# Performance work log

Measured on AMD Instinct MI355X. Metric: run time of the kernel, lower is better.

## Reference

```python
import jax, jax.numpy as jnp
import numpy as np
from jax.ops import segment_sum

N_NODES = 50000
N_EDGES = 800000
HIDDEN = 96
N_CLASSES = 10
N_GRAPHS = 64


def gcn_conv(x, W, b, src, dst, num_nodes):
    """PyG GCNConv: symmetric-normalized aggregation with self-loops.
    out = D^{-1/2} (A + I) D^{-1/2} (x W) + b, with D the degree of A + I.
    Self-loop contribution handled analytically instead of appending edges.
    """
    ones = jnp.ones((src.shape[0],), dtype=x.dtype)
    deg = segment_sum(ones, dst, num_segments=num_nodes) + 1.0  # +1 for self-loop
    dinv = jax.lax.rsqrt(deg)
    h = x @ W  # [N, H] small GEMM
    norm = dinv[src] * dinv[dst]  # [E]
    msg = h[src] * norm[:, None]  # [E, H] dominant gather
    out = segment_sum(msg, dst, num_segments=num_nodes)  # scatter-add
    out = out + h * (dinv * dinv)[:, None]  # self-loop term
    return out + b


def setup_inputs() -> dict:
    key = jax.random.key(0)
    ks = jax.random.split(key, 12)
    x = jax.random.normal(ks[0], (N_NODES, HIDDEN), dtype=jnp.float32)
    edge_index = jax.random.randint(ks[1], (2, N_EDGES), 0, N_NODES, dtype=jnp.int64)
    batch = jnp.sort(jax.random.randint(ks[2], (N_NODES,), 0, N_GRAPHS, dtype=jnp.int64))
    s = 1.0 / np.sqrt(HIDDEN)
    W0 = jax.random.normal(ks[3], (HIDDEN, HIDDEN), dtype=jnp.float32) * s
    b0 = jnp.zeros((HIDDEN,), dtype=jnp.float32)
    W1 = jax.random.normal(ks[4], (HIDDEN, HIDDEN), dtype=jnp.float32) * s
    b1 = jnp.zeros((HIDDEN,), dtype=jnp.float32)
    W2 = jax.random.normal(ks[5], (HIDDEN, HIDDEN), dtype=jnp.float32) * s
    b2 = jnp.zeros((HIDDEN,), dtype=jnp.float32)
    W_lin = jax.random.normal(ks[6], (HIDDEN, N_CLASSES), dtype=jnp.float32) * s
    b_lin = jnp.zeros((N_CLASSES,), dtype=jnp.float32)
    return {"x": x, "edge_index": edge_index, "batch": batch,
            "W0": W0, "b0": b0, "W1": W1, "b1": b1, "W2": W2, "b2": b2,
            "W_lin": W_lin, "b_lin": b_lin}


def reference(x, edge_index, batch, W0, b0, W1, b1, W2, b2, W_lin, b_lin):
    src, dst = edge_index[0], edge_index[1]
    n = x.shape[0]
    h = jax.nn.relu(gcn_conv(x, W0, b0, src, dst, n))
    h = jax.nn.relu(gcn_conv(h, W1, b1, src, dst, n))
    h = gcn_conv(h, W2, b2, src, dst, n)  # last layer: no activation
    # global_mean_pool over batch index
    sums = segment_sum(h, batch, num_segments=N_GRAPHS)  # [G, H]
    cnts = segment_sum(jnp.ones((n,), dtype=h.dtype), batch, num_segments=N_GRAPHS)
    pooled = sums / jnp.maximum(cnts, 1.0)[:, None]
    # dropout is identity in eval mode
    return pooled @ W_lin + b_lin  # [G, num_classes]
```

## Files before the change

kernel.cpp:

```cpp
#include <hip/hip_runtime.h>
#include <hip/hip_bf16.h>

#define HID 96
#define NGRAPHS 64
#define SENT 0xC3C3u
#define NROWS 50116

typedef __attribute__((ext_vector_type(8))) short short8;
typedef __attribute__((ext_vector_type(4))) float floatx4;
typedef __attribute__((ext_vector_type(8))) unsigned short ushort8v;

__device__ __forceinline__ float bf16_to_f32(unsigned short u) {
    unsigned int v = ((unsigned int)u) << 16;
    return __builtin_bit_cast(float, v);
}
__device__ __forceinline__ unsigned short f32_to_bf16(float f) {
    unsigned int u = __builtin_bit_cast(unsigned int, f);
    u += 0x7fff + ((u >> 16) & 1);
    return (unsigned short)(u >> 16);
}

__device__ __forceinline__ void gather_row(const unsigned short* __restrict__ h,
                                           const unsigned short* __restrict__ csr,
                                           int i, int end, int fi, float& a0,
                                           float& a1) {
    for (; i < end; i += 8) {
        ushort8v iv = *(const ushort8v*)(csr + i);
        ushort2 v0 = *(const ushort2*)(h + (size_t)iv[0] * HID + fi);
        ushort2 v1 = *(const ushort2*)(h + (size_t)iv[1] * HID + fi);
        ushort2 v2 = *(const ushort2*)(h + (size_t)iv[2] * HID + fi);
        ushort2 v3 = *(const ushort2*)(h + (size_t)iv[3] * HID + fi);
        ushort2 v4 = *(const ushort2*)(h + (size_t)iv[4] * HID + fi);
        ushort2 v5 = *(const ushort2*)(h + (size_t)iv[5] * HID + fi);
        ushort2 v6 = *(const ushort2*)(h + (size_t)iv[6] * HID + fi);
        ushort2 v7 = *(const ushort2*)(h + (size_t)iv[7] * HID + fi);
        a0 += bf16_to_f32(v0.x) + bf16_to_f32(v1.x) + bf16_to_f32(v2.x) +
              bf16_to_f32(v3.x) + bf16_to_f32(v4.x) + bf16_to_f32(v5.x) +
              bf16_to_f32(v6.x) + bf16_to_f32(v7.x);
        a1 += bf16_to_f32(v0.y) + bf16_to_f32(v1.y) + bf16_to_f32(v2.y) +
              bf16_to_f32(v3.y) + bf16_to_f32(v4.y) + bf16_to_f32(v5.y) +
              bf16_to_f32(v6.y) + bf16_to_f32(v7.y);
    }
}

__global__ void deg_kernel(const int* __restrict__ dst, int* __restrict__ deg,
                           int n_edges) {
    int t = blockIdx.x * blockDim.x + threadIdx.x;
    int e0 = t * 4;
    if (e0 + 4 <= n_edges) {
        int4 d4 = *(const int4*)(dst + e0);
        atomicAdd(&deg[d4.x], 1);
        atomicAdd(&deg[d4.y], 1);
        atomicAdd(&deg[d4.z], 1);
        atomicAdd(&deg[d4.w], 1);
    } else {
        for (int e = e0; e < n_edges; e++) atomicAdd(&deg[dst[e]], 1);
    }
}

__global__ __launch_bounds__(256) void scan_phaseA(const int* __restrict__ deg,
                                                   float* __restrict__ dinv,
                                                   int* __restrict__ blocksum,
                                                   int N) {
    int i = blockIdx.x * 256 + threadIdx.x;
    int d = (i < N) ? deg[i] : 0;
    if (i < N) dinv[i] = rsqrtf((float)d + 1.0f);
    int v = (d + 7) & ~7;
#pragma unroll
    for (int off = 32; off > 0; off >>= 1) v += __shfl_down(v, off, 64);
    __shared__ int s[4];
    if ((threadIdx.x & 63) == 0) s[threadIdx.x >> 6] = v;
    __syncthreads();
    if (threadIdx.x == 0) blocksum[blockIdx.x] = s[0] + s[1] + s[2] + s[3];
}

__global__ __launch_bounds__(256) void scan_phaseB(int* __restrict__ blocksum,
                                                   int* __restrict__ blockoff,
                                                   int nblocks) {
    __shared__ int s[256];
    int t = threadIdx.x;
    int own = (t < nblocks) ? blocksum[t] : 0;
    s[t] = own;
    __syncthreads();
#pragma unroll
    for (int off = 1; off < 256; off <<= 1) {
        int v = (t >= off) ? s[t - off] : 0;
        __syncthreads();
        s[t] += v;
        __syncthreads();
    }
    if (t < nblocks) blockoff[t] = s[t] - own;
}

__global__ __launch_bounds__(256) void scan_phaseC(const int* __restrict__ deg,
                                                   const int* __restrict__ blockoff,
                                                   int* __restrict__ rowptr,
                                                   int* __restrict__ cursor, int N) {
    __shared__ int s[256];
    int t = threadIdx.x;
    int i = blockIdx.x * 256 + t;
    int own = (i < N) ? (deg[i] + 7) & ~7 : 0;
    s[t] = own;
    __syncthreads();
#pragma unroll
    for (int off = 1; off < 256; off <<= 1) {
        int v = (t >= off) ? s[t - off] : 0;
        __syncthreads();
        s[t] += v;
        __syncthreads();
    }
    if (i < N) {
        int r = blockoff[blockIdx.x] + s[t] - own;
        rowptr[i] = r;
        cursor[i] = r;
        if (i == N - 1) rowptr[N] = r + own;
    }
}

__global__ void csr_fill(const int* __restrict__ src, const int* __restrict__ dst,
                         int* __restrict__ cursor,
                         unsigned short* __restrict__ csr_src, int n_edges) {
    int t = blockIdx.x * blockDim.x + threadIdx.x;
    int e0 = t * 4;
    if (e0 + 4 <= n_edges) {
        int4 d4 = *(const int4*)(dst + e0);
        int4 s4 = *(const int4*)(src + e0);
        int p0 = atomicAdd(&cursor[d4.x], 1);
        int p1 = atomicAdd(&cursor[d4.y], 1);
        int p2 = atomicAdd(&cursor[d4.z], 1);
        int p3 = atomicAdd(&cursor[d4.w], 1);
        csr_src[p0] = (unsigned short)s4.x;
        csr_src[p1] = (unsigned short)s4.y;
        csr_src[p2] = (unsigned short)s4.z;
        csr_src[p3] = (unsigned short)s4.w;
    } else {
        for (int e = e0; e < n_edges; e++) {
            int p = atomicAdd(&cursor[dst[e]], 1);
            csr_src[p] = (unsigned short)src[e];
        }
    }
}

__global__ void swizzle_W(const float* __restrict__ W0, const float* __restrict__ W1,
                          const float* __restrict__ W2, unsigned short* __restrict__ Wz) {
    const float* W = (blockIdx.x == 0) ? W0 : (blockIdx.x == 1) ? W1 : W2;
    unsigned short* dst = Wz + blockIdx.x * HID * HID;
    for (int e = threadIdx.x; e < HID * HID; e += blockDim.x) {
        int k = e / HID, n = e % HID;
        int nt = n >> 4, kki = k >> 5, quad = (k >> 3) & 3, j = k & 7;
        int lane = (n & 15) | (quad << 4);
        dst[(((nt * 3 + kki) * 64 + lane) << 3) | j] = f32_to_bf16(W[e]);
    }
}

__global__ void zero_sentinel(unsigned short* __restrict__ a,
                              unsigned short* __restrict__ b) {
    int t = threadIdx.x;
    a[(size_t)SENT * HID + t] = 0;
    b[(size_t)SENT * HID + t] = 0;
}

__global__ __launch_bounds__(256) void gemm0_f32(
    const float* __restrict__ X, const unsigned short* __restrict__ Wz,
    const float* __restrict__ dinv, unsigned short* __restrict__ Out, int Mtiles) {
    int wv = threadIdx.x >> 6;
    int lane = threadIdx.x & 63;
    int quad = lane >> 4;
    int mrow = lane & 15;
    int tt = blockIdx.x * 2 + (wv >> 1);
    int half = wv & 1;
    if (tt >= Mtiles) return;

    short8 bfrag[9];
    const short8* Wz8 = (const short8*)Wz;
#pragma unroll
    for (int f = 0; f < 9; f++) bfrag[f] = Wz8[(half * 9 + f) * 64 + lane];

    int m0 = tt * 16;
    const float* arow = X + (size_t)(m0 + mrow) * HID + quad * 8;
    short8 a[3];
#pragma unroll
    for (int kb = 0; kb < 3; kb++) {
        float4 u = *(const float4*)(arow + kb * 32);
        float4 v = *(const float4*)(arow + kb * 32 + 4);
        short8 t;
        t[0] = (short)f32_to_bf16(u.x); t[1] = (short)f32_to_bf16(u.y);
        t[2] = (short)f32_to_bf16(u.z); t[3] = (short)f32_to_bf16(u.w);
        t[4] = (short)f32_to_bf16(v.x); t[5] = (short)f32_to_bf16(v.y);
        t[6] = (short)f32_to_bf16(v.z); t[7] = (short)f32_to_bf16(v.w);
        a[kb] = t;
    }
    float dscale[4];
#pragma unroll
    for (int r = 0; r < 4; r++) dscale[r] = dinv[m0 + quad * 4 + r];
    unsigned short* orow = Out + (size_t)m0 * HID;
#pragma unroll
    for (int ntl = 0; ntl < 3; ntl++) {
        int nt = half * 3 + ntl;
        floatx4 c = {0.0f, 0.0f, 0.0f, 0.0f};
        c = __builtin_amdgcn_mfma_f32_16x16x32_bf16(a[0], bfrag[ntl * 3 + 0], c, 0, 0, 0);
        c = __builtin_amdgcn_mfma_f32_16x16x32_bf16(a[1], bfrag[ntl * 3 + 1], c, 0, 0, 0);
        c = __builtin_amdgcn_mfma_f32_16x16x32_bf16(a[2], bfrag[ntl * 3 + 2], c, 0, 0, 0);
#pragma unroll
        for (int r = 0; r < 4; r++)
            orow[(size_t)(quad * 4 + r) * HID + nt * 16 + mrow] =
                f32_to_bf16(c[r] * dscale[r]);
    }
}

__global__ __launch_bounds__(256) void fused_gather_gemm(
    const unsigned short* __restrict__ h, const int* __restrict__ rowptr,
    const unsigned short* __restrict__ csr, const float* __restrict__ dinv,
    const float* __restrict__ bias, const unsigned short* __restrict__ Wz,
    unsigned short* __restrict__ Out, int Mtiles) {
    __shared__ unsigned short tile[2][16][104];
    int wv = threadIdx.x >> 6;
    int lane = threadIdx.x & 63;
    int quad = lane >> 4;
    int mrow = lane & 15;
    int tsel = wv >> 1;
    int half = wv & 1;
    int tt = blockIdx.x * 2 + tsel;
    bool active = tt < Mtiles;
    int fi = (lane < 48) ? lane * 2 : 94;

    if (active) {
        float b0 = bias[fi], b1 = bias[fi + 1];
        int n0 = tt * 16;
        for (int j = half * 8; j < half * 8 + 8; j++) {
            int n = n0 + j;
            int i = rowptr[n];
            int end = rowptr[n + 1];
            float di = dinv[n];
            ushort2 hv = *(const ushort2*)(h + (size_t)n * HID + fi);
            float a0 = bf16_to_f32(hv.x);
            float a1 = bf16_to_f32(hv.y);
            gather_row(h, csr, i, end, fi, a0, a1);
            a0 = fmaxf(a0 * di + b0, 0.0f);
            a1 = fmaxf(a1 * di + b1, 0.0f);
            if (lane < 48) {
                tile[tsel][j][fi] = f32_to_bf16(a0);
                tile[tsel][j][fi + 1] = f32_to_bf16(a1);
            }
        }
    }
    __syncthreads();
    if (!active) return;

    short8 bfrag[9];
    const short8* Wz8 = (const short8*)Wz;
#pragma unroll
    for (int f = 0; f < 9; f++) bfrag[f] = Wz8[(half * 9 + f) * 64 + lane];

    const unsigned short* tp = &tile[tsel][0][0];
    short8 a[3];
#pragma unroll
    for (int kb = 0; kb < 3; kb++)
        a[kb] = *(const short8*)(tp + mrow * 104 + quad * 8 + kb * 32);
    int n0 = tt * 16;
    float dscale[4];
#pragma unroll
    for (int r = 0; r < 4; r++) dscale[r] = dinv[n0 + quad * 4 + r];
    unsigned short* orow = Out + (size_t)n0 * HID;
#pragma unroll
    for (int ntl = 0; ntl < 3; ntl++) {
        int nt = half * 3 + ntl;
        floatx4 c = {0.0f, 0.0f, 0.0f, 0.0f};
        c = __builtin_amdgcn_mfma_f32_16x16x32_bf16(a[0], bfrag[ntl * 3 + 0], c, 0, 0, 0);
        c = __builtin_amdgcn_mfma_f32_16x16x32_bf16(a[1], bfrag[ntl * 3 + 1], c, 0, 0, 0);
        c = __builtin_amdgcn_mfma_f32_16x16x32_bf16(a[2], bfrag[ntl * 3 + 2], c, 0, 0, 0);
#pragma unroll
        for (int r = 0; r < 4; r++)
            orow[(size_t)(quad * 4 + r) * HID + nt * 16 + mrow] =
                f32_to_bf16(c[r] * dscale[r]);
    }
}

__global__ __launch_bounds__(256) void gather_pool(
    const unsigned short* __restrict__ h, const int* __restrict__ rowptr,
    const unsigned short* __restrict__ csr, const float* __restrict__ dinv,
    const float* __restrict__ bias, const int* __restrict__ batch,
    float* __restrict__ psum, float* __restrict__ pcnt, int Ntiles8) {
    int wv = threadIdx.x >> 6;
    int lane = threadIdx.x & 63;
    int tt = blockIdx.x * 4 + wv;
    if (tt >= Ntiles8) return;
    int fi = (lane < 48) ? lane * 2 : 94;
    float b0 = bias[fi], b1 = bias[fi + 1];

    int n0 = tt * 8;
    int g_cur = batch[n0];
    float s0 = 0.0f, s1 = 0.0f;
    int cnt = 0;
    for (int j = 0; j < 8; j++) {
        int n = n0 + j;
        int i = rowptr[n];
        int end = rowptr[n + 1];
        float di = dinv[n];
        ushort2 hv = *(const ushort2*)(h + (size_t)n * HID + fi);
        float a0 = bf16_to_f32(hv.x);
        float a1 = bf16_to_f32(hv.y);
        gather_row(h, csr, i, end, fi, a0, a1);
        a0 = a0 * di + b0;
        a1 = a1 * di + b1;
        int g = batch[n];
        if (g != g_cur) {
            if (lane < 48) {
                atomicAdd(&psum[g_cur * HID + fi], s0);
                atomicAdd(&psum[g_cur * HID + fi + 1], s1);
            }
            if (lane == 0) atomicAdd(&pcnt[g_cur], (float)cnt);
            s0 = 0.0f; s1 = 0.0f; cnt = 0;
            g_cur = g;
        }
        s0 += a0;
        s1 += a1;
        cnt++;
    }
    if (lane < 48) {
        atomicAdd(&psum[g_cur * HID + fi], s0);
        atomicAdd(&psum[g_cur * HID + fi + 1], s1);
    }
    if (lane == 0) atomicAdd(&pcnt[g_cur], (float)cnt);
}

__global__ __launch_bounds__(640) void final_kernel(
    const float* __restrict__ sums, const float* __restrict__ cnts,
    const float* __restrict__ Wlin, const float* __restrict__ blin,
    float* __restrict__ out) {
    int t = threadIdx.x;
    if (t >= NGRAPHS * 10) return;
    int g = t / 10;
    int c = t % 10;
    float denom = fmaxf(cnts[g], 1.0f);
    float acc = blin[c];
#pragma unroll
    for (int f = 0; f < HID; f++)
        acc += (sums[g * HID + f] / denom) * Wlin[f * 10 + c];
    out[t] = acc;
}

extern "C" void kernel_launch(void* const* d_in, const int* in_sizes, int n_in,
                              void* d_out, int out_size, void* d_ws,
                              size_t ws_size, hipStream_t stream) {
    const float* x = (const float*)d_in[0];
    const int* edge = (const int*)d_in[1];
    const int* batch = (const int*)d_in[2];
    const float* W[3] = {(const float*)d_in[3], (const float*)d_in[5],
                         (const float*)d_in[7]};
    const float* B[3] = {(const float*)d_in[4], (const float*)d_in[6],
                         (const float*)d_in[8]};
    const float* Wlin = (const float*)d_in[9];
    const float* blin = (const float*)d_in[10];
    float* out = (float*)d_out;

    int N = in_sizes[0] / HID;
    int E = in_sizes[1] / 2;
    const int* src = edge;
    const int* dst = edge + E;
    int NB = (N + 255) / 256;

    char* ws = (char*)d_ws;
    size_t off = 0;
    auto alloc = [&](size_t bytes) {
        void* p = ws + off;
        off += (bytes + 255) & ~(size_t)255;
        return p;
    };
    int* deg = (int*)alloc((size_t)N * 4);
    float* dinv = (float*)alloc((size_t)N * 4);
    int* rowptr = (int*)alloc(((size_t)N + 1) * 4);
    int* cursor = (int*)alloc((size_t)N * 4);
    int* blocksum = (int*)alloc((size_t)NB * 4);
    int* blockoff = (int*)alloc((size_t)NB * 4);
    size_t csr_cap = (size_t)E + 8 * (size_t)N;
    unsigned short* csr_src = (unsigned short*)alloc(csr_cap * 2);
    unsigned short* Wz = (unsigned short*)alloc(3 * HID * HID * 2);
    unsigned short* bufA = (unsigned short*)alloc((size_t)NROWS * HID * 2);
    unsigned short* bufB = (unsigned short*)alloc((size_t)NROWS * HID * 2);
    float* psum = (float*)alloc((NGRAPHS * HID + NGRAPHS) * 4);
    float* pcnt = psum + NGRAPHS * HID;

    hipMemsetAsync(deg, 0, (size_t)N * 4, stream);
    hipMemsetAsync(csr_src, 0xC3, csr_cap * 2, stream);
    hipMemsetAsync(psum, 0, (NGRAPHS * HID + NGRAPHS) * 4, stream);
    deg_kernel<<<(E / 4 + 255) / 256, 256, 0, stream>>>(dst, deg, E);
    scan_phaseA<<<NB, 256, 0, stream>>>(deg, dinv, blocksum, N);
    scan_phaseB<<<1, 256, 0, stream>>>(blocksum, blockoff, NB);
    scan_phaseC<<<NB, 256, 0, stream>>>(deg, blockoff, rowptr, cursor, N);
    csr_fill<<<(E / 4 + 255) / 256, 256, 0, stream>>>(src, dst, cursor, csr_src, E);
    swizzle_W<<<3, 256, 0, stream>>>(W[0], W[1], W[2], Wz);
    zero_sentinel<<<1, HID, 0, stream>>>(bufA, bufB);

    int Mtiles = (N + 15) / 16;
    int grid2 = (Mtiles + 1) / 2;
    int Ntiles8 = (N + 7) / 8;
    int gridp = (Ntiles8 + 3) / 4;

    gemm0_f32<<<grid2, 256, 0, stream>>>(x, Wz, dinv, bufA, Mtiles);
    fused_gather_gemm<<<grid2, 256, 0, stream>>>(
        bufA, rowptr, csr_src, dinv, B[0], Wz + 1 * HID * HID, bufB, Mtiles);
    fused_gather_gemm<<<grid2, 256, 0, stream>>>(
        bufB, rowptr, csr_src, dinv, B[1], Wz + 2 * HID * HID, bufA, Mtiles);
    gather_pool<<<gridp, 256, 0, stream>>>(bufA, rowptr, csr_src, dinv, B[2],
                                           batch, psum, pcnt, Ntiles8);
    final_kernel<<<1, 640, 0, stream>>>(psum, pcnt, Wlin, blin, out);
}
```

Before: 324.0 us.

## Gather four rows per wave with 16-byte feature loads in CSR aggregation

The gather kernels now split each wave into four 16-lane groups, each handling a different node with 8 bf16 features per lane loaded as one 16-byte vector, instead of one node per wave with 2 features per lane. Padding uses a sentinel row and a wave-wide max length so that all groups iterate together. Pooling reduces the four rows across groups with shuffles before the atomics, and both kernels request two blocks per CU via launch bounds. This cuts per-edge load instruction count and latency chains, at the cost of wasted work when node degrees differ within a group and higher register pressure.

```diff
diff --git a/kernel.cpp b/kernel.cpp
--- a/kernel.cpp
+++ b/kernel.cpp
@@ -20,26 +20,21 @@
     return (unsigned short)(u >> 16);
 }
 
-__device__ __forceinline__ void gather_row(const unsigned short* __restrict__ h,
+__device__ __forceinline__ void gather4grp(const unsigned short* __restrict__ h,
                                            const unsigned short* __restrict__ csr,
-                                           int i, int end, int fi, float& a0,
-                                           float& a1) {
-    for (; i < end; i += 8) {
-        ushort8v iv = *(const ushort8v*)(csr + i);
-        ushort2 v0 = *(const ushort2*)(h + (size_t)iv[0] * HID + fi);
-        ushort2 v1 = *(const ushort2*)(h + (size_t)iv[1] * HID + fi);
-        ushort2 v2 = *(const ushort2*)(h + (size_t)iv[2] * HID + fi);
-        ushort2 v3 = *(const ushort2*)(h + (size_t)iv[3] * HID + fi);
-        ushort2 v4 = *(const ushort2*)(h + (size_t)iv[4] * HID + fi);
-        ushort2 v5 = *(const ushort2*)(h + (size_t)iv[5] * HID + fi);
-        ushort2 v6 = *(const ushort2*)(h + (size_t)iv[6] * HID + fi);
-        ushort2 v7 = *(const ushort2*)(h + (size_t)iv[7] * HID + fi);
-        a0 += bf16_to_f32(v0.x) + bf16_to_f32(v1.x) + bf16_to_f32(v2.x) +
-              bf16_to_f32(v3.x) + bf16_to_f32(v4.x) + bf16_to_f32(v5.x) +
-              bf16_to_f32(v6.x) + bf16_to_f32(v7.x);
-        a1 += bf16_to_f32(v0.y) + bf16_to_f32(v1.y) + bf16_to_f32(v2.y) +
-              bf16_to_f32(v3.y) + bf16_to_f32(v4.y) + bf16_to_f32(v5.y) +
-              bf16_to_f32(v6.y) + bf16_to_f32(v7.y);
+                                           int start, int plen, int maxlen,
+                                           int ceff, float* a ) {
+    for (int i = 0; i < maxlen; i += 8) {
+        int off = min(i, plen - 8);
+        off = max(off, 0);
+        ushort8v iv = *(const ushort8v*)(csr + start + off);
+#pragma unroll
+        for (int k = 0; k < 8; k++) {
+            int s = (i + k < plen) ? (int)iv[k] : (int)SENT;
+            ushort8v rv = *(const ushort8v*)(h + (size_t)s * HID + ceff * 8);
+#pragma unroll
+            for (int t = 0; t < 8; t++) a[t] += bf16_to_f32(rv[t]);
+        }
     }
 }
 
@@ -208,7 +203,7 @@
     }
 }
 
-__global__ __launch_bounds__(256) void fused_gather_gemm(
+__global__ __launch_bounds__(256, 2) void fused_gather_gemm(
     const unsigned short* __restrict__ h, const int* __restrict__ rowptr,
     const unsigned short* __restrict__ csr, const float* __restrict__ dinv,
     const float* __restrict__ bias, const unsigned short* __restrict__ Wz,
@@ -222,26 +217,39 @@
     int half = wv & 1;
     int tt = blockIdx.x * 2 + tsel;
     bool active = tt < Mtiles;
-    int fi = (lane < 48) ? lane * 2 : 94;
+    int g = lane >> 4;
+    int c = lane & 15;
+    int ceff = min(c, 11);
 
     if (active) {
-        float b0 = bias[fi], b1 = bias[fi + 1];
+        float bb[8];
+        {
+            float4 bl = *(const float4*)(bias + ceff * 8);
+            float4 bh = *(const float4*)(bias + ceff * 8 + 4);
+            bb[0] = bl.x; bb[1] = bl.y; bb[2] = bl.z; bb[3] = bl.w;
+            bb[4] = bh.x; bb[5] = bh.y; bb[6] = bh.z; bb[7] = bh.w;
+        }
         int n0 = tt * 16;
-        for (int j = half * 8; j < half * 8 + 8; j++) {
+#pragma unroll
+        for (int pass = 0; pass < 2; pass++) {
+            int j = half * 8 + pass * 4 + g;
             int n = n0 + j;
-            int i = rowptr[n];
-            int end = rowptr[n + 1];
+            int start = rowptr[n];
+            int plen = rowptr[n + 1] - start;
             float di = dinv[n];
-            ushort2 hv = *(const ushort2*)(h + (size_t)n * HID + fi);
-            float a0 = bf16_to_f32(hv.x);
-            float a1 = bf16_to_f32(hv.y);
-            gather_row(h, csr, i, end, fi, a0, a1);
-            a0 = fmaxf(a0 * di + b0, 0.0f);
-            a1 = fmaxf(a1 * di + b1, 0.0f);
-            if (lane < 48) {
-                tile[tsel][j][fi] = f32_to_bf16(a0);
-                tile[tsel][j][fi + 1] = f32_to_bf16(a1);
-            }
+            ushort8v hv = *(const ushort8v*)(h + (size_t)n * HID + ceff * 8);
+            float a[8];
+#pragma unroll
+            for (int t = 0; t < 8; t++) a[t] = bf16_to_f32(hv[t]);
+            int m = plen;
+            m = max(m, __shfl_xor(m, 16));
+            m = max(m, __shfl_xor(m, 32));
+            gather4grp(h, csr, start, plen, m, ceff, a);
+            ushort8v o;
+#pragma unroll
+            for (int t = 0; t < 8; t++)
+                o[t] = f32_to_bf16(fmaxf(a[t] * di + bb[t], 0.0f));
+            if (c < 12) *(ushort8v*)(&tile[tsel][j][c * 8]) = o;
         }
     }
     __syncthreads();
@@ -265,18 +273,31 @@
 #pragma unroll
     for (int ntl = 0; ntl < 3; ntl++) {
         int nt = half * 3 + ntl;
-        floatx4 c = {0.0f, 0.0f, 0.0f, 0.0f};
-        c = __builtin_amdgcn_mfma_f32_16x16x32_bf16(a[0], bfrag[ntl * 3 + 0], c, 0, 0, 0);
-        c = __builtin_amdgcn_mfma_f32_16x16x32_bf16(a[1], bfrag[ntl * 3 + 1], c, 0, 0, 0);
-        c = __builtin_amdgcn_mfma_f32_16x16x32_bf16(a[2], bfrag[ntl * 3 + 2], c, 0, 0, 0);
+        floatx4 cc = {0.0f, 0.0f, 0.0f, 0.0f};
+        cc = __builtin_amdgcn_mfma_f32_16x16x32_bf16(a[0], bfrag[ntl * 3 + 0], cc, 0, 0, 0);
+        cc = __builtin_amdgcn_mfma_f32_16x16x32_bf16(a[1], bfrag[ntl * 3 + 1], cc, 0, 0, 0);
+        cc = __builtin_amdgcn_mfma_f32_16x16x32_bf16(a[2], bfrag[ntl * 3 + 2], cc, 0, 0, 0);
 #pragma unroll
         for (int r = 0; r < 4; r++)
             orow[(size_t)(quad * 4 + r) * HID + nt * 16 + mrow] =
-                f32_to_bf16(c[r] * dscale[r]);
-    }
-}
-
-__global__ __launch_bounds__(256) void gather_pool(
+                f32_to_bf16(cc[r] * dscale[r]);
+    }
+}
+
+__device__ __forceinline__ void pool_flush(int g, int c, int lane, int g_cur,
+                                           const float* run, int cnt,
+                                           float* __restrict__ psum,
+                                           float* __restrict__ pcnt) {
+    if (cnt == 0) return;
+    if (g == 0 && c < 12) {
+#pragma unroll
+        for (int t = 0; t < 8; t++)
+            atomicAdd(&psum[g_cur * HID + c * 8 + t], run[t]);
+    }
+    if (lane == 0) atomicAdd(&pcnt[g_cur], (float)cnt);
+}
+
+__global__ __launch_bounds__(256, 2) void gather_pool(
     const unsigned short* __restrict__ h, const int* __restrict__ rowptr,
     const unsigned short* __restrict__ csr, const float* __restrict__ dinv,
     const float* __restrict__ bias, const int* __restrict__ batch,
@@ -285,43 +306,76 @@
     int lane = threadIdx.x & 63;
     int tt = blockIdx.x * 4 + wv;
     if (tt >= Ntiles8) return;
-    int fi = (lane < 48) ? lane * 2 : 94;
-    float b0 = bias[fi], b1 = bias[fi + 1];
+    int g = lane >> 4;
+    int c = lane & 15;
+    int ceff = min(c, 11);
+    float bb[8];
+    {
+        float4 bl = *(const float4*)(bias + ceff * 8);
+        float4 bh = *(const float4*)(bias + ceff * 8 + 4);
+        bb[0] = bl.x; bb[1] = bl.y; bb[2] = bl.z; bb[3] = bl.w;
+        bb[4] = bh.x; bb[5] = bh.y; bb[6] = bh.z; bb[7] = bh.w;
+    }
 
     int n0 = tt * 8;
     int g_cur = batch[n0];
-    float s0 = 0.0f, s1 = 0.0f;
+    float run[8] = {0, 0, 0, 0, 0, 0, 0, 0};
     int cnt = 0;
-    for (int j = 0; j < 8; j++) {
-        int n = n0 + j;
-        int i = rowptr[n];
-        int end = rowptr[n + 1];
+#pragma unroll
+    for (int pass = 0; pass < 2; pass++) {
+        int nbase = n0 + pass * 4;
+        int n = nbase + g;
+        int start = rowptr[n];
+        int plen = rowptr[n + 1] - start;
         float di = dinv[n];
-        ushort2 hv = *(const ushort2*)(h + (size_t)n * HID + fi);
-        float a0 = bf16_to_f32(hv.x);
-        float a1 = bf16_to_f32(hv.y);
-        gather_row(h, csr, i, end, fi, a0, a1);
-        a0 = a0 * di + b0;
-        a1 = a1 * di + b1;
-        int g = batch[n];
-        if (g != g_cur) {
-            if (lane < 48) {
-                atomicAdd(&psum[g_cur * HID + fi], s0);
-                atomicAdd(&psum[g_cur * HID + fi + 1], s1);
+        ushort8v hv = *(const ushort8v*)(h + (size_t)n * HID + ceff * 8);
+        float a[8];
+#pragma unroll
+        for (int t = 0; t < 8; t++) a[t] = bf16_to_f32(hv[t]);
+        int m = plen;
+        m = max(m, __shfl_xor(m, 16));
+        m = max(m, __shfl_xor(m, 32));
+        gather4grp(h, csr, start, plen, m, ceff, a);
+#pragma unroll
+        for (int t = 0; t < 8; t++) a[t] = a[t] * di + bb[t];
+
+        int gfirst = batch[nbase];
+        int glast = batch[nbase + 3];
+        if (gfirst == glast) {
+            float r[8];
+#pragma unroll
+            for (int t = 0; t < 8; t++) {
+                float v = a[t];
+                v += __shfl_xor(v, 16);
+                v += __shfl_xor(v, 32);
+                r[t] = v;
             }
-            if (lane == 0) atomicAdd(&pcnt[g_cur], (float)cnt);
-            s0 = 0.0f; s1 = 0.0f; cnt = 0;
-            g_cur = g;
+            if (gfirst != g_cur) {
+                pool_flush(g, c, lane, g_cur, run, cnt, psum, pcnt);
+#pragma unroll
+                for (int t = 0; t < 8; t++) run[t] = 0.0f;
+                cnt = 0;
+                g_cur = gfirst;
+            }
+#pragma unroll
+            for (int t = 0; t < 8; t++) run[t] += r[t];
+            cnt += 4;
+        } else {
+            pool_flush(g, c, lane, g_cur, run, cnt, psum, pcnt);
+#pragma unroll
+            for (int t = 0; t < 8; t++) run[t] = 0.0f;
+            cnt = 0;
+            int gp = batch[n];
+            if (c < 12) {
+#pragma unroll
+                for (int t = 0; t < 8; t++)
+                    atomicAdd(&psum[gp * HID + c * 8 + t], a[t]);
+            }
+            if (c == 0) atomicAdd(&pcnt[gp], 1.0f);
+            g_cur = glast;
         }
-        s0 += a0;
-        s1 += a1;
-        cnt++;
-    }
-    if (lane < 48) {
-        atomicAdd(&psum[g_cur * HID + fi], s0);
-        atomicAdd(&psum[g_cur * HID + fi + 1], s1);
-    }
-    if (lane == 0) atomicAdd(&pcnt[g_cur], (float)cnt);
+    }
+    pool_flush(g, c, lane, g_cur, run, cnt, psum, pcnt);
 }
 
 __global__ __launch_bounds__(640) void final_kernel(
```

Result: slower. 335.9 us (+3.6%).
